# Performance work log

Measured on AMD Instinct MI355X. Metric: run time of the kernel, lower is better.

Reference implementation:

```python
import jax, jax.numpy as jnp
import numpy as np

B, L, D = 4, 2048, 1024
E, K, H = 8, 2, 4096      # num_experts, top_k, expert hidden (mlp_ratio=4)
HS = 4096                 # shared expert hidden (n_shared_experts=1 * 4*D)
EPS = 1e-6


def setup_inputs() -> dict:
    key = jax.random.key(0)
    ks = jax.random.split(key, 12)
    s = 0.02
    return {
        "x": jax.random.normal(ks[0], (B, L, D), jnp.float32),
        "time_c": jax.random.normal(ks[1], (B, D), jnp.float32),
        # AdaptiveLayerNorm: cond -> (shift, scale)
        "ada_w": jax.random.normal(ks[2], (D, 2 * D), jnp.float32) * s,
        "ada_b": jnp.zeros((2 * D,), jnp.float32),
        # router gate
        "gate_w": jax.random.normal(ks[3], (D, E), jnp.float32) * s,
        # routed experts (stacked)
        "w1": jax.random.normal(ks[4], (E, D, H), jnp.float32) * s,
        "b1": jnp.zeros((E, H), jnp.float32),
        "w2": jax.random.normal(ks[5], (E, H, D), jnp.float32) * s,
        "b2": jnp.zeros((E, D), jnp.float32),
        # shared expert
        "sw1": jax.random.normal(ks[6], (D, HS), jnp.float32) * s,
        "sb1": jnp.zeros((HS,), jnp.float32),
        "sw2": jax.random.normal(ks[7], (HS, D), jnp.float32) * s,
        "sb2": jnp.zeros((D,), jnp.float32),
    }


def _forward(x, time_c, ada_w, ada_b, gate_w, w1, b1, w2, b2, sw1, sb1, sw2, sb2):
    # --- AdaptiveLayerNorm: LN (no affine) modulated by time condition ---
    mu = jnp.mean(x, axis=-1, keepdims=True)
    var = jnp.var(x, axis=-1, keepdims=True)
    ln = (x - mu) * jax.lax.rsqrt(var + EPS)                       # (B,L,D)
    cond = jax.nn.silu(time_c) @ ada_w + ada_b                     # (B,2D)
    shift, scale = jnp.split(cond, 2, axis=-1)                     # (B,D) each
    xn = ln * (1.0 + scale[:, None, :]) + shift[:, None, :]        # (B,L,D)

    # --- SparseMoeBlock ---
    t = xn.reshape(B * L, D)                                       # (T,D) tokens
    probs = jax.nn.softmax(t @ gate_w, axis=-1)                    # (T,E)
    topv, topi = jax.lax.top_k(probs, K)                           # (T,K)
    topv = topv / jnp.sum(topv, axis=-1, keepdims=True)            # renormalize
    # dense per-expert combine weights via one-hot scatter: (T,E)
    w_dense = jnp.sum(jax.nn.one_hot(topi, E, dtype=t.dtype) * topv[..., None], axis=1)

    # shared expert applied to every token
    y = jax.nn.gelu(t @ sw1 + sb1) @ sw2 + sb2                     # (T,D)
    # routed experts: weighted combine (loop over fixed small E)
    for e in range(E):
        h = jax.nn.gelu(t @ w1[e] + b1[e])                         # (T,H)
        y = y + w_dense[:, e:e + 1] * (h @ w2[e] + b2[e])

    return x + y.reshape(B, L, D)                                  # residual


def reference(x, time_c, ada_w, ada_b, gate_w, w1, b1, w2, b2, sw1, sb1, sw2, sb2):
    return _forward(x, time_c, ada_w, ada_b, gate_w, w1, b1, w2, b2, sw1, sb1, sw2, sb2)
```

## Files before the change

### kernel.cpp

```cpp
#include <hip/hip_runtime.h>
#include <hip/hip_bf16.h>
#include <cstdint>

#define T_TOKENS 8192
#define DMODEL   1024
#define DHID     4096
#define NEXP     8

typedef float  f32x4  __attribute__((ext_vector_type(4)));
typedef __bf16 bf16x8 __attribute__((ext_vector_type(8)));

__device__ __forceinline__ void async_copy16(const void* gp, void* lp) {
    __builtin_amdgcn_global_load_lds(
        (const __attribute__((address_space(1))) void*)gp,
        (__attribute__((address_space(3))) void*)lp, 16, 0, 0);
}

__device__ __forceinline__ float gelu_tanh(float x) {
    float u = 0.7978845608028654f * (x + 0.044715f * x * x * x);
    return 0.5f * x * (1.0f + tanhf(u));
}

__global__ void transpose_cvt(const float* __restrict__ src,
                              __hip_bfloat16* __restrict__ dst, int R, int C) {
    __shared__ float tile[32][33];
    int bz = blockIdx.z;
    const float* s = src + (size_t)bz * R * C;
    __hip_bfloat16* d = dst + (size_t)bz * R * C;
    int c0 = blockIdx.x * 32, r0 = blockIdx.y * 32;
    int tx = threadIdx.x, ty = threadIdx.y;
#pragma unroll
    for (int i = 0; i < 4; i++) {
        int r = r0 + ty + i * 8;
        tile[ty + i * 8][tx] = s[(size_t)r * C + c0 + tx];
    }
    __syncthreads();
#pragma unroll
    for (int i = 0; i < 4; i++) {
        int c = c0 + ty + i * 8;
        d[(size_t)c * R + r0 + tx] = __float2bfloat16(tile[tx][ty + i * 8]);
    }
}

__global__ void cond_kernel(const float* __restrict__ time_c,
                            const float* __restrict__ ada_w,
                            const float* __restrict__ ada_b,
                            float* __restrict__ cond) {
    __shared__ float sl[DMODEL];
    int b = blockIdx.x >> 3;
    int j = ((blockIdx.x & 7) << 8) + threadIdx.x;
    for (int i = threadIdx.x; i < DMODEL; i += 256) {
        float tc = time_c[b * DMODEL + i];
        sl[i] = tc / (1.0f + __expf(-tc));
    }
    __syncthreads();
    float acc = ada_b[j];
    for (int i = 0; i < DMODEL; i++)
        acc += sl[i] * ada_w[(size_t)i * 2048 + j];
    cond[b * 2048 + j] = acc;
}

__global__ __launch_bounds__(256) void ln_gate_kernel(
    const float* __restrict__ x, const float* __restrict__ cond,
    const float* __restrict__ gate_w,
    __hip_bfloat16* __restrict__ xnb,
    int* __restrict__ topi, float* __restrict__ topw, int* __restrict__ counts) {
    int t = blockIdx.x;
    int b = t >> 11;
    int tid = threadIdx.x, lane = tid & 63, wave = tid >> 6;
    const float4* xr = (const float4*)(x + (size_t)t * DMODEL);
    float4 v = xr[tid];
    float s = v.x + v.y + v.z + v.w;
    float q = v.x * v.x + v.y * v.y + v.z * v.z + v.w * v.w;
#pragma unroll
    for (int o = 32; o > 0; o >>= 1) {
        s += __shfl_down(s, o, 64);
        q += __shfl_down(q, o, 64);
    }
    __shared__ float red[8];
    if (lane == 0) { red[wave] = s; red[4 + wave] = q; }
    __syncthreads();
    float tsum = red[0] + red[1] + red[2] + red[3];
    float tsq  = red[4] + red[5] + red[6] + red[7];
    float mu   = tsum * (1.0f / DMODEL);
    float var  = tsq * (1.0f / DMODEL) - mu * mu;
    float rstd = rsqrtf(var + 1e-6f);

    int j = tid * 4;
    const float4* cb = (const float4*)(cond + (size_t)b * 2048);
    float4 sh = cb[tid];
    float4 sc = cb[256 + tid];
    float xv[4];
    xv[0] = (v.x - mu) * rstd * (1.0f + sc.x) + sh.x;
    xv[1] = (v.y - mu) * rstd * (1.0f + sc.y) + sh.y;
    xv[2] = (v.z - mu) * rstd * (1.0f + sc.z) + sh.z;
    xv[3] = (v.w - mu) * rstd * (1.0f + sc.w) + sh.w;
    union { ushort4 u4; __hip_bfloat16 h[4]; } pk;
#pragma unroll
    for (int r = 0; r < 4; r++) pk.h[r] = __float2bfloat16(xv[r]);
    *((ushort4*)(xnb + (size_t)t * DMODEL + j)) = pk.u4;

    float g[8] = {0, 0, 0, 0, 0, 0, 0, 0};
    const float4* gw = (const float4*)gate_w;
#pragma unroll
    for (int r = 0; r < 4; r++) {
        float4 ga = gw[(j + r) * 2];
        float4 gb = gw[(j + r) * 2 + 1];
        g[0] += xv[r] * ga.x; g[1] += xv[r] * ga.y;
        g[2] += xv[r] * ga.z; g[3] += xv[r] * ga.w;
        g[4] += xv[r] * gb.x; g[5] += xv[r] * gb.y;
        g[6] += xv[r] * gb.z; g[7] += xv[r] * gb.w;
    }
#pragma unroll
    for (int e = 0; e < 8; e++) {
#pragma unroll
        for (int o = 32; o > 0; o >>= 1) g[e] += __shfl_down(g[e], o, 64);
    }
    __shared__ float gred[4][8];
    if (lane == 0) {
#pragma unroll
        for (int e = 0; e < 8; e++) gred[wave][e] = g[e];
    }
    __syncthreads();
    if (tid == 0) {
        float l[8];
#pragma unroll
        for (int e = 0; e < 8; e++)
            l[e] = gred[0][e] + gred[1][e] + gred[2][e] + gred[3][e];
        int i0 = 0; float v0 = l[0];
        int i1 = -1; float v1 = -3.4e38f;
        for (int e = 1; e < 8; e++) {
            if (l[e] > v0) { v1 = v0; i1 = i0; v0 = l[e]; i0 = e; }
            else if (l[e] > v1) { v1 = l[e]; i1 = e; }
        }
        float r = __expf(v1 - v0);
        float w0 = 1.0f / (1.0f + r);
        topi[2 * t] = i0; topi[2 * t + 1] = i1;
        topw[2 * t] = w0; topw[2 * t + 1] = 1.0f - w0;
        atomicAdd(&counts[i0], 1);
        atomicAdd(&counts[i1], 1);
    }
}

__global__ void scan_kernel(const int* __restrict__ counts,
                            int* __restrict__ offs, int* __restrict__ cursors) {
    if (threadIdx.x == 0) {
        int a = 0;
        for (int e = 0; e < NEXP; e++) { offs[e] = a; cursors[e] = a; a += counts[e]; }
    }
}

__global__ void fill_kernel(const int* __restrict__ topi, const float* __restrict__ topw,
                            int* __restrict__ cursors,
                            int* __restrict__ rowlist, float* __restrict__ wlist,
                            int* __restrict__ slots) {
    int t = blockIdx.x * 256 + threadIdx.x;
#pragma unroll
    for (int k = 0; k < 2; k++) {
        int e = topi[2 * t + k];
        int pos = atomicAdd(&cursors[e], 1);
        rowlist[pos] = t;
        wlist[pos] = topw[2 * t + k];
        slots[2 * t + k] = pos;
    }
}

__global__ __launch_bounds__(256) void combine_kernel(
    const int* __restrict__ slots, const float* __restrict__ yr,
    float* __restrict__ out) {
    int t = blockIdx.x;
    int p0 = slots[2 * t], p1 = slots[2 * t + 1];
    int i = threadIdx.x;
    const float4* a = (const float4*)(yr + (size_t)p0 * DMODEL);
    const float4* b = (const float4*)(yr + (size_t)p1 * DMODEL);
    float4* o = (float4*)(out + (size_t)t * DMODEL);
    float4 va = a[i], vb = b[i], vo = o[i];
    vo.x += va.x + vb.x;
    vo.y += va.y + vb.y;
    vo.z += va.z + vb.z;
    vo.w += va.w + vb.w;
    o[i] = vo;
}

template <int MODE>
__global__ __launch_bounds__(256, 4) void gemm_bt(
    const __hip_bfloat16* __restrict__ A,
    const __hip_bfloat16* __restrict__ Bt,
    const float* __restrict__ bias,
    const float* __restrict__ xres,
    float* __restrict__ outf,
    __hip_bfloat16* __restrict__ outb,
    const int* __restrict__ rowlist,
    const float* __restrict__ wlist,
    const int* __restrict__ offs,
    const int* __restrict__ counts,
    int K, int N) {
    int e = 0, seg_off = 0, Mcnt = 0;
    if constexpr (MODE >= 2) {
        e = blockIdx.z;
        Mcnt = counts[e];
        if ((int)blockIdx.x * 128 >= Mcnt) return;
        seg_off = offs[e];
    }
    const __hip_bfloat16* Bte = Bt + (size_t)e * (size_t)N * K;
    const float* biase = bias + (size_t)e * N;
    int row0 = blockIdx.x * 128, col0 = blockIdx.y * 128;

    __shared__ __align__(16) __hip_bfloat16 sA[128 * 64];
    __shared__ __align__(16) __hip_bfloat16 sB[128 * 64];

    int tid = threadIdx.x, wave = tid >> 6, lane = tid & 63;
    int wm = wave >> 1, wn = wave & 1;

    int kc = ((lane & 7) ^ (lane >> 3)) * 8;
    const __hip_bfloat16* aptr[4];
    const __hip_bfloat16* bptr[4];
#pragma unroll
    for (int i = 0; i < 4; i++) {
        int c = wave * 4 + i;
        int rr = c * 8 + (lane >> 3);
        size_t arow;
        if constexpr (MODE == 0 || MODE == 1) {
            arow = (size_t)(row0 + rr);
        } else {
            int p = row0 + rr; if (p > Mcnt - 1) p = Mcnt - 1;
            arow = (MODE == 2) ? (size_t)rowlist[seg_off + p] : (size_t)(seg_off + p);
        }
        aptr[i] = A + arow * K + kc;
        int nn = col0 + c * 8 + (lane >> 3);
        bptr[i] = Bte + (size_t)nn * K + kc;
    }

    f32x4 acc[4][4];
#pragma unroll
    for (int tm = 0; tm < 4; tm++)
#pragma unroll
        for (int tn = 0; tn < 4; tn++) acc[tm][tn] = (f32x4){0.f, 0.f, 0.f, 0.f};

    char* sAc = (char*)&sA[0];
    char* sBc = (char*)&sB[0];

    for (int k0 = 0; k0 < K; k0 += 64) {
#pragma unroll
        for (int i = 0; i < 4; i++) {
            int c = wave * 4 + i;
            async_copy16(aptr[i], sAc + c * 1024);
            async_copy16(bptr[i], sBc + c * 1024);
            aptr[i] += 64;
            bptr[i] += 64;
        }
        asm volatile("s_waitcnt vmcnt(0)" ::: "memory");
        __syncthreads();
        const short* sa = (const short*)sAc;
        const short* sb = (const short*)sBc;
#pragma unroll
        for (int kk = 0; kk < 64; kk += 32) {
            int kbc = (kk >> 3) + (lane >> 4);
            int swz = ((kbc ^ (lane & 7)) << 3);
            bf16x8 af[4], bfr[4];
#pragma unroll
            for (int tm = 0; tm < 4; tm++)
                af[tm] = *(const bf16x8*)(sa + (size_t)(wm * 64 + tm * 16 + (lane & 15)) * 64 + swz);
#pragma unroll
            for (int tn = 0; tn < 4; tn++)
                bfr[tn] = *(const bf16x8*)(sb + (size_t)(wn * 64 + tn * 16 + (lane & 15)) * 64 + swz);
#pragma unroll
            for (int tm = 0; tm < 4; tm++)
#pragma unroll
                for (int tn = 0; tn < 4; tn++)
                    acc[tm][tn] = __builtin_amdgcn_mfma_f32_16x16x32_bf16(
                        af[tm], bfr[tn], acc[tm][tn], 0, 0, 0);
        }
        __syncthreads();
    }

#pragma unroll
    for (int tm = 0; tm < 4; tm++) {
        int rbase = wm * 64 + tm * 16 + ((lane >> 4) << 2);
        float wv[4];
        if constexpr (MODE == 3) {
#pragma unroll
            for (int i = 0; i < 4; i++) {
                int p = row0 + rbase + i;
                wv[i] = (p < Mcnt) ? wlist[seg_off + p] : 0.0f;
            }
        }
#pragma unroll
        for (int tn = 0; tn < 4; tn++) {
            int c = col0 + wn * 64 + tn * 16 + (lane & 15);
            float bb = biase[c];
#pragma unroll
            for (int i = 0; i < 4; i++) {
                int rl = rbase + i;
                float v = acc[tm][tn][i] + bb;
                if constexpr (MODE == 0) {
                    outb[(size_t)(row0 + rl) * N + c] = __float2bfloat16(gelu_tanh(v));
                } else if constexpr (MODE == 1) {
                    size_t idx = (size_t)(row0 + rl) * N + c;
                    outf[idx] = xres[idx] + v;
                } else if constexpr (MODE == 2) {
                    int p = row0 + rl;
                    if (p < Mcnt)
                        outb[(size_t)(seg_off + p) * N + c] = __float2bfloat16(gelu_tanh(v));
                } else {
                    int p = row0 + rl;
                    if (p < Mcnt)
                        outf[(size_t)(seg_off + p) * N + c] = wv[i] * v;
                }
            }
        }
    }
}

extern "C" void kernel_launch(void* const* d_in, const int* in_sizes, int n_in,
                              void* d_out, int out_size, void* d_ws, size_t ws_size,
                              hipStream_t stream) {
    const float* x      = (const float*)d_in[0];
    const float* time_c = (const float*)d_in[1];
    const float* ada_w  = (const float*)d_in[2];
    const float* ada_b  = (const float*)d_in[3];
    const float* gate_w = (const float*)d_in[4];
    const float* w1     = (const float*)d_in[5];
    const float* b1     = (const float*)d_in[6];
    const float* w2     = (const float*)d_in[7];
    const float* b2     = (const float*)d_in[8];
    const float* sw1    = (const float*)d_in[9];
    const float* sb1    = (const float*)d_in[10];
    const float* sw2    = (const float*)d_in[11];
    const float* sb2    = (const float*)d_in[12];
    float* out = (float*)d_out;
    (void)in_sizes; (void)n_in; (void)out_size; (void)ws_size;

    char* ws = (char*)d_ws;
    size_t off = 0;
    auto alloc = [&](size_t bytes) -> char* {
        char* p = ws + off;
        off += (bytes + 255) & ~(size_t)255;
        return p;
    };
    __hip_bfloat16* xnb  = (__hip_bfloat16*)alloc((size_t)T_TOKENS * DMODEL * 2);
    __hip_bfloat16* w1t  = (__hip_bfloat16*)alloc((size_t)NEXP * DMODEL * DHID * 2);
    __hip_bfloat16* w2t  = (__hip_bfloat16*)alloc((size_t)NEXP * DMODEL * DHID * 2);
    __hip_bfloat16* sw1t = (__hip_bfloat16*)alloc((size_t)DMODEL * DHID * 2);
    __hip_bfloat16* sw2t = (__hip_bfloat16*)alloc((size_t)DMODEL * DHID * 2);
    __hip_bfloat16* hs   = (__hip_bfloat16*)alloc((size_t)T_TOKENS * DHID * 2);
    __hip_bfloat16* hr   = (__hip_bfloat16*)alloc((size_t)2 * T_TOKENS * DHID * 2);
    float* cond    = (float*)alloc(4 * 2048 * 4);
    int*   topi    = (int*)alloc(T_TOKENS * 2 * 4);
    float* topw    = (float*)alloc(T_TOKENS * 2 * 4);
    int*   rowlist = (int*)alloc(2 * T_TOKENS * 4);
    float* wlist   = (float*)alloc(2 * T_TOKENS * 4);
    int*   slots   = (int*)alloc(2 * T_TOKENS * 4);
    int*   counts  = (int*)alloc(256);
    int*   offs    = (int*)alloc(256);
    int*   cursors = (int*)alloc(256);
    float* yr = (float*)hs;

    hipMemsetAsync(counts, 0, NEXP * sizeof(int), stream);

    dim3 tb(32, 8);
    transpose_cvt<<<dim3(128, 32, 8), tb, 0, stream>>>(w1, w1t, 1024, 4096);
    transpose_cvt<<<dim3(32, 128, 8), tb, 0, stream>>>(w2, w2t, 4096, 1024);
    transpose_cvt<<<dim3(128, 32, 1), tb, 0, stream>>>(sw1, sw1t, 1024, 4096);
    transpose_cvt<<<dim3(32, 128, 1), tb, 0, stream>>>(sw2, sw2t, 4096, 1024);

    cond_kernel<<<32, 256, 0, stream>>>(time_c, ada_w, ada_b, cond);
    ln_gate_kernel<<<T_TOKENS, 256, 0, stream>>>(x, cond, gate_w, xnb, topi, topw, counts);
    scan_kernel<<<1, 64, 0, stream>>>(counts, offs, cursors);
    fill_kernel<<<32, 256, 0, stream>>>(topi, topw, cursors, rowlist, wlist, slots);

    gemm_bt<0><<<dim3(64, 32), 256, 0, stream>>>(xnb, sw1t, sb1, nullptr, nullptr, hs,
                                                 nullptr, nullptr, nullptr, nullptr, 1024, 4096);
    gemm_bt<1><<<dim3(64, 8), 256, 0, stream>>>(hs, sw2t, sb2, x, out, nullptr,
                                                nullptr, nullptr, nullptr, nullptr, 4096, 1024);
    gemm_bt<2><<<dim3(64, 32, 8), 256, 0, stream>>>(xnb, w1t, b1, nullptr, nullptr, hr,
                                                    rowlist, nullptr, offs, counts, 1024, 4096);
    gemm_bt<3><<<dim3(64, 8, 8), 256, 0, stream>>>(hr, w2t, b2, nullptr, yr, nullptr,
                                                   nullptr, wlist, offs, counts, 4096, 1024);
    combine_kernel<<<T_TOKENS, 256, 0, stream>>>(slots, yr, out);
}
```

Baseline: 1.523 ms.

## Double-buffer GEMM shared-memory tiles and use exp-based GELU

The GEMM main loop now uses two LDS buffers for A and B. The next K-tile is prefetched with async global-to-LDS copies while MFMAs run on the current tile, which hides global load latency behind compute. LDS use doubles to 64KB per block and launch bounds drop from 4 to 2 blocks per SM, so occupancy goes down. GELU's tanh form is also rewritten with the algebraically equivalent x*sigmoid(2u) using __expf, a cheaper epilogue op.

```diff
diff --git a/kernel.cpp b/kernel.cpp
--- a/kernel.cpp
+++ b/kernel.cpp
@@ -17,8 +17,8 @@
 }
 
 __device__ __forceinline__ float gelu_tanh(float x) {
-    float u = 0.7978845608028654f * (x + 0.044715f * x * x * x);
-    return 0.5f * x * (1.0f + tanhf(u));
+    float z = x * (1.5957691216057308f + 0.07135481283247289f * x * x);
+    return x / (1.0f + __expf(-z));
 }
 
 __global__ void transpose_cvt(const float* __restrict__ src,
@@ -183,7 +183,7 @@
 }
 
 template <int MODE>
-__global__ __launch_bounds__(256, 4) void gemm_bt(
+__global__ __launch_bounds__(256, 2) void gemm_bt(
     const __hip_bfloat16* __restrict__ A,
     const __hip_bfloat16* __restrict__ Bt,
     const float* __restrict__ bias,
@@ -206,8 +206,8 @@
     const float* biase = bias + (size_t)e * N;
     int row0 = blockIdx.x * 128, col0 = blockIdx.y * 128;
 
-    __shared__ __align__(16) __hip_bfloat16 sA[128 * 64];
-    __shared__ __align__(16) __hip_bfloat16 sB[128 * 64];
+    __shared__ __align__(16) __hip_bfloat16 sA[2][128 * 64];
+    __shared__ __align__(16) __hip_bfloat16 sB[2][128 * 64];
 
     int tid = threadIdx.x, wave = tid >> 6, lane = tid & 63;
     int wm = wave >> 1, wn = wave & 1;
@@ -237,22 +237,37 @@
 #pragma unroll
         for (int tn = 0; tn < 4; tn++) acc[tm][tn] = (f32x4){0.f, 0.f, 0.f, 0.f};
 
-    char* sAc = (char*)&sA[0];
-    char* sBc = (char*)&sB[0];
-
-    for (int k0 = 0; k0 < K; k0 += 64) {
-#pragma unroll
-        for (int i = 0; i < 4; i++) {
-            int c = wave * 4 + i;
-            async_copy16(aptr[i], sAc + c * 1024);
-            async_copy16(bptr[i], sBc + c * 1024);
-            aptr[i] += 64;
-            bptr[i] += 64;
-        }
-        asm volatile("s_waitcnt vmcnt(0)" ::: "memory");
-        __syncthreads();
-        const short* sa = (const short*)sAc;
-        const short* sb = (const short*)sBc;
+    char* sAc = (char*)&sA[0][0];
+    char* sBc = (char*)&sB[0][0];
+
+    int nt = K >> 6;
+#pragma unroll
+    for (int i = 0; i < 4; i++) {
+        int c = wave * 4 + i;
+        async_copy16(aptr[i], sAc + c * 1024);
+        async_copy16(bptr[i], sBc + c * 1024);
+        aptr[i] += 64;
+        bptr[i] += 64;
+    }
+    asm volatile("s_waitcnt vmcnt(0)" ::: "memory");
+    __syncthreads();
+
+    int cur = 0;
+    for (int t = 0; t < nt; ++t) {
+        if (t + 1 < nt) {
+            char* dA = (char*)&sA[cur ^ 1][0];
+            char* dB = (char*)&sB[cur ^ 1][0];
+#pragma unroll
+            for (int i = 0; i < 4; i++) {
+                int c = wave * 4 + i;
+                async_copy16(aptr[i], dA + c * 1024);
+                async_copy16(bptr[i], dB + c * 1024);
+                aptr[i] += 64;
+                bptr[i] += 64;
+            }
+        }
+        const short* sa = (const short*)&sA[cur][0];
+        const short* sb = (const short*)&sB[cur][0];
 #pragma unroll
         for (int kk = 0; kk < 64; kk += 32) {
             int kbc = (kk >> 3) + (lane >> 4);
@@ -271,7 +286,11 @@
                     acc[tm][tn] = __builtin_amdgcn_mfma_f32_16x16x32_bf16(
                         af[tm], bfr[tn], acc[tm][tn], 0, 0, 0);
         }
-        __syncthreads();
+        if (t + 1 < nt) {
+            asm volatile("s_waitcnt vmcnt(0)" ::: "memory");
+            __syncthreads();
+        }
+        cur ^= 1;
     }
 
 #pragma unroll
```

After: 1.749 ms. 1.15x slower.
